# Performance work log

Hardware: AMD Instinct MI355X
Metric: run time of the kernel (lower is better)

Reference implementation:

```python
import jax, jax.numpy as jnp
import numpy as np

N_HEADS = 16

def setup_inputs() -> dict:
    key = jax.random.key(0)
    ks = jax.random.split(key, 8)
    bs, t, h, dh = 32, 512, 1024, 64
    s = lambda k, shape: jax.random.normal(k, shape, dtype=jnp.float32) * 0.02
    return {
        "x": jax.random.normal(ks[0], (bs, t, h), dtype=jnp.float32),
        "Wq": s(ks[1], (h, h)),
        "bq": s(ks[2], (h,)),
        "Wk": s(ks[3], (h, h)),
        "bk": s(ks[4], (h,)),
        "Wv": s(ks[5], (h, dh)),
        "bv": s(ks[6], (dh,)),
        "Wo": s(ks[7], (dh, h)),
    }

def reference(x, Wq, bq, Wk, bk, Wv, bv, Wo):
    bs, t, h = x.shape
    dh = Wv.shape[1]
    nh = N_HEADS
    # projections (context == x; static_features=None path)
    q = (x @ Wq + bq).reshape(bs, t, nh, dh)   # [b,t,h,d]
    k = (x @ Wk + bk).reshape(bs, t, nh, dh)
    v = x @ Wv + bv                             # shared single-head V: [b,t,d]
    scale = dh ** -0.5
    # per-head scores [b,h,q,k]
    score = jnp.einsum('bqhd,bkhd->bhqk', q, k) * scale
    # causal mask (mask_future_timesteps=True): -inf above diagonal
    mask = jnp.triu(jnp.full((t, t), -jnp.inf, dtype=score.dtype), 1)
    score = score + mask
    prob = jax.nn.softmax(score, axis=-1)       # attn_dropout is identity (p=0)
    # broadcast shared V across heads
    attn_vec = jnp.einsum('bhqk,bkd->bhqd', prob, v)   # [b,h,t,d]
    m_attn_vec = jnp.mean(attn_vec, axis=1)            # head-mean pooling [b,t,d]
    out = m_attn_vec @ Wo                              # out_proj, no bias; out_dropout identity
    return out, attn_vec
```

## Files before the change

### kernel.cpp

```cpp
#include <hip/hip_runtime.h>
#include <hip/hip_bf16.h>
#include <math.h>

#define BS 32
#define TT 512
#define HH 1024
#define NH 16
#define DH 64
#define MM (BS*TT)
#define NCAT 2176

typedef __attribute__((ext_vector_type(8))) __bf16 bf16x8;
typedef __attribute__((ext_vector_type(4))) float  f32x4;

#define QSCALE 0.18033688011112042f

__device__ __forceinline__ void gld16(const void* g, void* l) {
    __builtin_amdgcn_global_load_lds(
        (const __attribute__((address_space(1))) unsigned int*)g,
        (__attribute__((address_space(3))) unsigned int*)l,
        16, 0, 0);
}

__global__ __launch_bounds__(256) void cvt_x(const float* __restrict__ x,
                                             __bf16* __restrict__ xb)
{
    const size_t i = ((size_t)blockIdx.x * 256 + threadIdx.x) * 8;
    float4 a = *(const float4*)(x + i);
    float4 b = *(const float4*)(x + i + 4);
    bf16x8 v;
    v[0] = (__bf16)a.x; v[1] = (__bf16)a.y; v[2] = (__bf16)a.z; v[3] = (__bf16)a.w;
    v[4] = (__bf16)b.x; v[5] = (__bf16)b.y; v[6] = (__bf16)b.z; v[7] = (__bf16)b.w;
    *(bf16x8*)(xb + i) = v;
}

__global__ __launch_bounds__(256) void prep_w(
    const float* __restrict__ Wq, const float* __restrict__ Wk,
    const float* __restrict__ Wv, const float* __restrict__ bq_,
    const float* __restrict__ bk_, const float* __restrict__ bv_,
    __bf16* __restrict__ Wt, float* __restrict__ bias_cat)
{
    __shared__ __align__(16) __bf16 tile[64][72];
    const int tid = threadIdx.x;
    const int n0 = blockIdx.x * 64;
    const int k0 = blockIdx.y * 64;

    const int n_l = tid & 63;
    const int k_b = tid >> 6;
    const int n   = n0 + n_l;
    #pragma unroll
    for (int j = 0; j < 16; ++j) {
        const int k_l = j * 4 + k_b;
        const int k   = k0 + k_l;
        float v;
        if (n < 1024)      v = Wq[(size_t)k * 1024 + n];
        else if (n < 2048) v = Wk[(size_t)k * 1024 + (n - 1024)];
        else if (n < 2112) v = Wv[(size_t)k * 64 + (n - 2048)];
        else               v = 0.f;
        tile[n_l][k_l] = (__bf16)v;
    }
    if (blockIdx.y == 0 && tid < 64) {
        const int nn = n0 + tid;
        bias_cat[nn] = (nn < 1024) ? bq_[nn]
                     : (nn < 2048) ? bk_[nn - 1024]
                     : (nn < 2112) ? bv_[nn - 2048] : 0.f;
    }
    __syncthreads();
    const int n_l2 = tid >> 2;
    const int k_l2 = (tid & 3) * 16;
    __bf16* dst = Wt + (size_t)(n0 + n_l2) * 1024 + k0 + k_l2;
    *(bf16x8*)dst       = *(const bf16x8*)&tile[n_l2][k_l2];
    *(bf16x8*)(dst + 8) = *(const bf16x8*)&tile[n_l2][k_l2 + 8];
}

__global__ __launch_bounds__(256) void gemm_qkv(
    const __bf16* __restrict__ A, const __bf16* __restrict__ B,
    const float* __restrict__ bias_cat,
    __bf16* __restrict__ Qo, __bf16* __restrict__ Ko,
    __bf16* __restrict__ Vt)
{
    __shared__ __align__(16) __bf16 sA[128 * 32];
    __shared__ __align__(16) __bf16 sB[128 * 32];

    const int tid  = threadIdx.x;
    const int wv   = tid >> 6;
    const int ln   = tid & 63;
    const int quad = ln >> 4;
    const int l16  = ln & 15;
    const int m0 = blockIdx.y * 128;
    const int n0 = blockIdx.x * 128;

    const int rw = (wv & 1) * 64;
    const int cw = (wv >> 1) * 64;

    f32x4 acc[4][4];
    #pragma unroll
    for (int i = 0; i < 4; ++i)
        #pragma unroll
        for (int j = 0; j < 4; ++j) acc[i][j] = f32x4{0, 0, 0, 0};

    const int srow = wv * 16 + (ln >> 2);
    const int scol = (ln & 3) * 8;
    const __bf16* ga0 = A + (size_t)(m0 + srow) * 1024 + scol;
    const __bf16* gb0 = B + (size_t)(n0 + srow) * 1024 + scol;
    __bf16* la0 = sA + wv * 512;
    __bf16* lb0 = sB + wv * 512;

    for (int k0 = 0; k0 < 1024; k0 += 32) {
        gld16(ga0 + k0, la0);
        gld16(ga0 + (size_t)64 * 1024 + k0, la0 + 2048);
        gld16(gb0 + k0, lb0);
        gld16(gb0 + (size_t)64 * 1024 + k0, lb0 + 2048);
        __syncthreads();

        bf16x8 af[4], bfr[4];
        #pragma unroll
        for (int mt = 0; mt < 4; ++mt)
            af[mt] = *(const bf16x8*)&sA[(rw + mt * 16 + l16) * 32 + quad * 8];
        #pragma unroll
        for (int nt = 0; nt < 4; ++nt)
            bfr[nt] = *(const bf16x8*)&sB[(cw + nt * 16 + l16) * 32 + quad * 8];
        #pragma unroll
        for (int mt = 0; mt < 4; ++mt)
            #pragma unroll
            for (int nt = 0; nt < 4; ++nt)
                acc[mt][nt] = __builtin_amdgcn_mfma_f32_16x16x32_bf16(af[mt], bfr[nt], acc[mt][nt], 0, 0, 0);
        __syncthreads();
    }

    #pragma unroll
    for (int mt = 0; mt < 4; ++mt) {
        #pragma unroll
        for (int nt = 0; nt < 4; ++nt) {
            const int colb = n0 + cw + nt * 16 + l16;
            if (colb >= 2112) continue;
            const float bias = bias_cat[colb];
            #pragma unroll
            for (int r = 0; r < 4; ++r) {
                const int row = m0 + rw + mt * 16 + quad * 4 + r;
                const int b = row >> 9, t = row & 511;
                float v = acc[mt][nt][r] + bias;
                if (colb < 1024) {
                    const int h = colb >> 6, d = colb & 63;
                    Qo[(((size_t)(b * NH + h) * TT) + t) * DH + d] = (__bf16)(v * QSCALE);
                } else if (colb < 2048) {
                    const int c = colb - 1024;
                    const int h = c >> 6, d = c & 63;
                    Ko[(((size_t)(b * NH + h) * TT) + t) * DH + d] = (__bf16)v;
                } else {
                    const int d = colb - 2048;
                    Vt[((size_t)(b * DH + d)) * TT + t] = (__bf16)v;
                }
            }
        }
    }
}

__global__ __launch_bounds__(256) void zero_mav(float* __restrict__ p)
{
    ((float4*)p)[(size_t)blockIdx.x * 256 + threadIdx.x] = float4{0, 0, 0, 0};
}

__global__ __launch_bounds__(256) void attn_mfma(
    const __bf16* __restrict__ Q, const __bf16* __restrict__ K,
    const __bf16* __restrict__ Vt, float* __restrict__ attn_vec,
    float* __restrict__ mav)
{
    const int wave = threadIdx.x >> 6;
    const int lane = threadIdx.x & 63;
    const int wid  = blockIdx.x * 4 + wave;
    const int qt2  = wid & 15;
    const int bh   = wid >> 4;
    const int b    = bh >> 4;
    const int q0   = qt2 << 5;
    const int quad = lane >> 4;
    const int l16  = lane & 15;

    const __bf16* Qbh = Q  + (size_t)bh * TT * DH;
    const __bf16* Kbh = K  + (size_t)bh * TT * DH;
    const __bf16* Vb  = Vt + (size_t)b  * DH * TT;

    const bf16x8 qA_lo = *(const bf16x8*)(Qbh + (size_t)(q0 + l16) * DH + quad * 8);
    const bf16x8 qA_hi = *(const bf16x8*)(Qbh + (size_t)(q0 + l16) * DH + 32 + quad * 8);
    const bf16x8 qB_lo = *(const bf16x8*)(Qbh + (size_t)(q0 + 16 + l16) * DH + quad * 8);
    const bf16x8 qB_hi = *(const bf16x8*)(Qbh + (size_t)(q0 + 16 + l16) * DH + 32 + quad * 8);

    const int perm = ((l16 >> 2) << 3) + (l16 & 3);
    const __bf16* kp1 = Kbh + (size_t)perm * DH;
    const __bf16* kp2 = Kbh + (size_t)(perm + 4) * DH;

    f32x4 OA[4] = {f32x4{0,0,0,0}, f32x4{0,0,0,0}, f32x4{0,0,0,0}, f32x4{0,0,0,0}};
    f32x4 OB[4] = {f32x4{0,0,0,0}, f32x4{0,0,0,0}, f32x4{0,0,0,0}, f32x4{0,0,0,0}};
    float lA = 0.f, lB = 0.f;

    const int kend = q0 + 32;

    bf16x8 k1a = *(const bf16x8*)(kp1 + quad * 8);
    bf16x8 k1b = *(const bf16x8*)(kp1 + 32 + quad * 8);
    bf16x8 k2a = *(const bf16x8*)(kp2 + quad * 8);
    bf16x8 k2b = *(const bf16x8*)(kp2 + 32 + quad * 8);

    for (int kb0 = 0; kb0 < kend; kb0 += 32) {
        const __bf16* vp = Vb + (size_t)l16 * TT + kb0 + quad * 8;
        bf16x8 vf0 = *(const bf16x8*)(vp);
        bf16x8 vf1 = *(const bf16x8*)(vp + (size_t)16 * TT);
        bf16x8 vf2 = *(const bf16x8*)(vp + (size_t)32 * TT);
        bf16x8 vf3 = *(const bf16x8*)(vp + (size_t)48 * TT);

        f32x4 s1A = __builtin_amdgcn_mfma_f32_16x16x32_bf16(k1a, qA_lo, f32x4{0,0,0,0}, 0, 0, 0);
        s1A       = __builtin_amdgcn_mfma_f32_16x16x32_bf16(k1b, qA_hi, s1A, 0, 0, 0);
        f32x4 s2A = __builtin_amdgcn_mfma_f32_16x16x32_bf16(k2a, qA_lo, f32x4{0,0,0,0}, 0, 0, 0);
        s2A       = __builtin_amdgcn_mfma_f32_16x16x32_bf16(k2b, qA_hi, s2A, 0, 0, 0);
        f32x4 s1B = __builtin_amdgcn_mfma_f32_16x16x32_bf16(k1a, qB_lo, f32x4{0,0,0,0}, 0, 0, 0);
        s1B       = __builtin_amdgcn_mfma_f32_16x16x32_bf16(k1b, qB_hi, s1B, 0, 0, 0);
        f32x4 s2B = __builtin_amdgcn_mfma_f32_16x16x32_bf16(k2a, qB_lo, f32x4{0,0,0,0}, 0, 0, 0);
        s2B       = __builtin_amdgcn_mfma_f32_16x16x32_bf16(k2b, qB_hi, s2B, 0, 0, 0);

        {
            const int kbn = (kb0 + 32 < kend) ? kb0 + 32 : kb0;
            const __bf16* nk1 = kp1 + (size_t)kbn * DH;
            const __bf16* nk2 = kp2 + (size_t)kbn * DH;
            k1a = *(const bf16x8*)(nk1 + quad * 8);
            k1b = *(const bf16x8*)(nk1 + 32 + quad * 8);
            k2a = *(const bf16x8*)(nk2 + quad * 8);
            k2b = *(const bf16x8*)(nk2 + 32 + quad * 8);
        }

        if (kb0 == q0) {
            const int qqA = q0 + l16, qqB = q0 + 16 + l16;
            #pragma unroll
            for (int r = 0; r < 4; ++r) {
                const int key1 = kb0 + quad * 8 + r;
                const int key2 = key1 + 4;
                if (key1 > qqA) s1A[r] = -INFINITY;
                if (key2 > qqA) s2A[r] = -INFINITY;
                if (key1 > qqB) s1B[r] = -INFINITY;
                if (key2 > qqB) s2B[r] = -INFINITY;
            }
        }

        bf16x8 pfA, pfB;
        float psA = 0.f, psB = 0.f;
        #pragma unroll
        for (int r = 0; r < 4; ++r) {
            float pa0 = exp2f(s1A[r]);
            float pa1 = exp2f(s2A[r]);
            float pb0 = exp2f(s1B[r]);
            float pb1 = exp2f(s2B[r]);
            psA += pa0 + pa1;
            psB += pb0 + pb1;
            pfA[r]     = (__bf16)pa0;
            pfA[4 + r] = (__bf16)pa1;
            pfB[r]     = (__bf16)pb0;
            pfB[4 + r] = (__bf16)pb1;
        }
        lA += psA;
        lB += psB;

        OA[0] = __builtin_amdgcn_mfma_f32_16x16x32_bf16(pfA, vf0, OA[0], 0, 0, 0);
        OB[0] = __builtin_amdgcn_mfma_f32_16x16x32_bf16(pfB, vf0, OB[0], 0, 0, 0);
        OA[1] = __builtin_amdgcn_mfma_f32_16x16x32_bf16(pfA, vf1, OA[1], 0, 0, 0);
        OB[1] = __builtin_amdgcn_mfma_f32_16x16x32_bf16(pfB, vf1, OB[1], 0, 0, 0);
        OA[2] = __builtin_amdgcn_mfma_f32_16x16x32_bf16(pfA, vf2, OA[2], 0, 0, 0);
        OB[2] = __builtin_amdgcn_mfma_f32_16x16x32_bf16(pfB, vf2, OB[2], 0, 0, 0);
        OA[3] = __builtin_amdgcn_mfma_f32_16x16x32_bf16(pfA, vf3, OA[3], 0, 0, 0);
        OB[3] = __builtin_amdgcn_mfma_f32_16x16x32_bf16(pfB, vf3, OB[3], 0, 0, 0);
    }

    lA += __shfl_xor(lA, 16);
    lA += __shfl_xor(lA, 32);
    lB += __shfl_xor(lB, 16);
    lB += __shfl_xor(lB, 32);

    #pragma unroll
    for (int r = 0; r < 4; ++r) {
        const float invA = 1.0f / __shfl(lA, quad * 4 + r);
        const float invB = 1.0f / __shfl(lB, quad * 4 + r);
        const int tA = q0 + quad * 4 + r;
        const int tB = tA + 16;
        float* opA = attn_vec + ((size_t)bh * TT + tA) * DH + l16;
        float* opB = attn_vec + ((size_t)bh * TT + tB) * DH + l16;
        float* mpA = mav + ((size_t)(b * TT + tA)) * DH + l16;
        float* mpB = mav + ((size_t)(b * TT + tB)) * DH + l16;
        #pragma unroll
        for (int nt = 0; nt < 4; ++nt) {
            const float vA = OA[nt][r] * invA;
            const float vB = OB[nt][r] * invB;
            opA[nt * 16] = vA;
            opB[nt * 16] = vB;
            atomicAdd(mpA + nt * 16, vA * (1.f / 16.f));
            atomicAdd(mpB + nt * 16, vB * (1.f / 16.f));
        }
    }
}

__global__ __launch_bounds__(256) void gemm_out(
    const float* __restrict__ A, const float* __restrict__ B,
    float* __restrict__ C, int M, int N, int K)
{
    __shared__ __align__(16) __bf16 sA[64][32];
    __shared__ __align__(16) __bf16 sB[64][32];

    const int tid  = threadIdx.x;
    const int wave = tid >> 6;
    const int lane = tid & 63;
    const int m0 = blockIdx.y * 64;
    const int n0 = blockIdx.x * 64;

    f32x4 acc[4] = {f32x4{0,0,0,0}, f32x4{0,0,0,0}, f32x4{0,0,0,0}, f32x4{0,0,0,0}};

    const int ar = tid >> 2;
    const int ac = (tid & 3) * 8;
    const int bk = tid >> 3;
    const int bc = (tid & 7) * 8;
    const int quad = lane >> 4;
    const int l16  = lane & 15;

    for (int k0 = 0; k0 < K; k0 += 32) {
        const float* ap = A + (size_t)(m0 + ar) * K + k0 + ac;
        float4 a0 = *(const float4*)ap;
        float4 a1 = *(const float4*)(ap + 4);
        {
            bf16x8 av;
            av[0] = (__bf16)a0.x; av[1] = (__bf16)a0.y; av[2] = (__bf16)a0.z; av[3] = (__bf16)a0.w;
            av[4] = (__bf16)a1.x; av[5] = (__bf16)a1.y; av[6] = (__bf16)a1.z; av[7] = (__bf16)a1.w;
            *(bf16x8*)&sA[ar][ac] = av;
        }
        const float* bp = B + (size_t)(k0 + bk) * N + n0 + bc;
        float4 b0 = *(const float4*)bp;
        float4 b1 = *(const float4*)(bp + 4);
        sB[bc + 0][bk] = (__bf16)b0.x;
        sB[bc + 1][bk] = (__bf16)b0.y;
        sB[bc + 2][bk] = (__bf16)b0.z;
        sB[bc + 3][bk] = (__bf16)b0.w;
        sB[bc + 4][bk] = (__bf16)b1.x;
        sB[bc + 5][bk] = (__bf16)b1.y;
        sB[bc + 6][bk] = (__bf16)b1.z;
        sB[bc + 7][bk] = (__bf16)b1.w;
        __syncthreads();

        bf16x8 afrag = *(const bf16x8*)&sA[wave * 16 + l16][quad * 8];
        #pragma unroll
        for (int tn = 0; tn < 4; ++tn) {
            bf16x8 bfrag = *(const bf16x8*)&sB[tn * 16 + l16][quad * 8];
            acc[tn] = __builtin_amdgcn_mfma_f32_16x16x32_bf16(afrag, bfrag, acc[tn], 0, 0, 0);
        }
        __syncthreads();
    }

    #pragma unroll
    for (int tn = 0; tn < 4; ++tn) {
        #pragma unroll
        for (int r = 0; r < 4; ++r) {
            int row = m0 + wave * 16 + quad * 4 + r;
            int col = n0 + tn * 16 + l16;
            C[(size_t)row * N + col] = acc[tn][r];
        }
    }
}

extern "C" void kernel_launch(void* const* d_in, const int* in_sizes, int n_in,
                              void* d_out, int out_size, void* d_ws, size_t ws_size,
                              hipStream_t stream)
{
    const float* x  = (const float*)d_in[0];
    const float* Wq = (const float*)d_in[1];
    const float* bq = (const float*)d_in[2];
    const float* Wk = (const float*)d_in[3];
    const float* bk = (const float*)d_in[4];
    const float* Wv = (const float*)d_in[5];
    const float* bv = (const float*)d_in[6];
    const float* Wo = (const float*)d_in[7];

    float* out      = (float*)d_out;
    float* attn_vec = out + (size_t)MM * HH;

    char* ws = (char*)d_ws;
    __bf16* xb  = (__bf16*)ws;
    __bf16* Wt  = xb + (size_t)MM * HH;
    float* bias_cat = (float*)(Wt + (size_t)NCAT * HH);
    __bf16* Qb  = (__bf16*)(bias_cat + 2304);
    __bf16* Kb  = Qb + (size_t)MM * HH;
    __bf16* Vt  = Kb + (size_t)MM * HH;
    float*  mav = (float*)xb;

    cvt_x<<<MM * HH / (256 * 8), 256, 0, stream>>>(x, xb);
    prep_w<<<dim3(NCAT / 64, HH / 64), 256, 0, stream>>>(Wq, Wk, Wv, bq, bk, bv, Wt, bias_cat);
    gemm_qkv<<<dim3(NCAT / 128, MM / 128), 256, 0, stream>>>(xb, Wt, bias_cat, Qb, Kb, Vt);
    zero_mav<<<(MM * DH / 4) / 256, 256, 0, stream>>>(mav);
    attn_mfma<<<(BS * NH * TT / 32) / 4, 256, 0, stream>>>(Qb, Kb, Vt, attn_vec, mav);
    gemm_out<<<dim3(HH / 64, MM / 64), 256, 0, stream>>>(mav, Wo, out, MM, HH, DH);
}
```

Baseline: 437.2 us.

## Reduce head-mean in shared memory with all heads per block, pair causal tiles

The attention kernel now launches one 1024-thread block per (batch, tile pair), with 16 waves covering the 16 heads. Each wave processes two query tiles, q-tile p and 15-p, to balance causal work. The head-mean is accumulated with LDS atomics into a shared buffer and written once with plain stores, so the zero_mav kernel and the global atomics go away. In exchange, the grid has fewer, larger blocks (256 blocks of 1024 threads), which may hurt occupancy and latency hiding. Each wave also now runs its two tiles one after the other.

```diff
diff --git a/kernel.cpp b/kernel.cpp
--- a/kernel.cpp
+++ b/kernel.cpp
@@ -156,141 +156,162 @@
     }
 }
 
-__global__ __launch_bounds__(256) void zero_mav(float* __restrict__ p)
-{
-    ((float4*)p)[(size_t)blockIdx.x * 256 + threadIdx.x] = float4{0, 0, 0, 0};
-}
-
-__global__ __launch_bounds__(256) void attn_mfma(
+__global__ __launch_bounds__(1024) void attn_mfma(
     const __bf16* __restrict__ Q, const __bf16* __restrict__ K,
     const __bf16* __restrict__ Vt, float* __restrict__ attn_vec,
     float* __restrict__ mav)
 {
+    __shared__ float smav[64][65];
+
     const int wave = threadIdx.x >> 6;
     const int lane = threadIdx.x & 63;
-    const int wid  = blockIdx.x * 4 + wave;
-    const int qt2  = wid & 15;
-    const int bh   = wid >> 4;
-    const int b    = bh >> 4;
-    const int q0   = qt2 << 5;
+    const int pair = blockIdx.x & 7;
+    const int b    = blockIdx.x >> 3;
+    const int bh   = b * NH + wave;
     const int quad = lane >> 4;
     const int l16  = lane & 15;
+
+    {
+        float* p = &smav[0][0];
+        for (int i = threadIdx.x; i < 64 * 65; i += 1024) p[i] = 0.f;
+    }
+    __syncthreads();
 
     const __bf16* Qbh = Q  + (size_t)bh * TT * DH;
     const __bf16* Kbh = K  + (size_t)bh * TT * DH;
     const __bf16* Vb  = Vt + (size_t)b  * DH * TT;
 
-    const bf16x8 qA_lo = *(const bf16x8*)(Qbh + (size_t)(q0 + l16) * DH + quad * 8);
-    const bf16x8 qA_hi = *(const bf16x8*)(Qbh + (size_t)(q0 + l16) * DH + 32 + quad * 8);
-    const bf16x8 qB_lo = *(const bf16x8*)(Qbh + (size_t)(q0 + 16 + l16) * DH + quad * 8);
-    const bf16x8 qB_hi = *(const bf16x8*)(Qbh + (size_t)(q0 + 16 + l16) * DH + 32 + quad * 8);
-
     const int perm = ((l16 >> 2) << 3) + (l16 & 3);
     const __bf16* kp1 = Kbh + (size_t)perm * DH;
     const __bf16* kp2 = Kbh + (size_t)(perm + 4) * DH;
 
-    f32x4 OA[4] = {f32x4{0,0,0,0}, f32x4{0,0,0,0}, f32x4{0,0,0,0}, f32x4{0,0,0,0}};
-    f32x4 OB[4] = {f32x4{0,0,0,0}, f32x4{0,0,0,0}, f32x4{0,0,0,0}, f32x4{0,0,0,0}};
-    float lA = 0.f, lB = 0.f;
-
-    const int kend = q0 + 32;
-
-    bf16x8 k1a = *(const bf16x8*)(kp1 + quad * 8);
-    bf16x8 k1b = *(const bf16x8*)(kp1 + 32 + quad * 8);
-    bf16x8 k2a = *(const bf16x8*)(kp2 + quad * 8);
-    bf16x8 k2b = *(const bf16x8*)(kp2 + 32 + quad * 8);
-
-    for (int kb0 = 0; kb0 < kend; kb0 += 32) {
-        const __bf16* vp = Vb + (size_t)l16 * TT + kb0 + quad * 8;
-        bf16x8 vf0 = *(const bf16x8*)(vp);
-        bf16x8 vf1 = *(const bf16x8*)(vp + (size_t)16 * TT);
-        bf16x8 vf2 = *(const bf16x8*)(vp + (size_t)32 * TT);
-        bf16x8 vf3 = *(const bf16x8*)(vp + (size_t)48 * TT);
-
-        f32x4 s1A = __builtin_amdgcn_mfma_f32_16x16x32_bf16(k1a, qA_lo, f32x4{0,0,0,0}, 0, 0, 0);
-        s1A       = __builtin_amdgcn_mfma_f32_16x16x32_bf16(k1b, qA_hi, s1A, 0, 0, 0);
-        f32x4 s2A = __builtin_amdgcn_mfma_f32_16x16x32_bf16(k2a, qA_lo, f32x4{0,0,0,0}, 0, 0, 0);
-        s2A       = __builtin_amdgcn_mfma_f32_16x16x32_bf16(k2b, qA_hi, s2A, 0, 0, 0);
-        f32x4 s1B = __builtin_amdgcn_mfma_f32_16x16x32_bf16(k1a, qB_lo, f32x4{0,0,0,0}, 0, 0, 0);
-        s1B       = __builtin_amdgcn_mfma_f32_16x16x32_bf16(k1b, qB_hi, s1B, 0, 0, 0);
-        f32x4 s2B = __builtin_amdgcn_mfma_f32_16x16x32_bf16(k2a, qB_lo, f32x4{0,0,0,0}, 0, 0, 0);
-        s2B       = __builtin_amdgcn_mfma_f32_16x16x32_bf16(k2b, qB_hi, s2B, 0, 0, 0);
-
-        {
-            const int kbn = (kb0 + 32 < kend) ? kb0 + 32 : kb0;
-            const __bf16* nk1 = kp1 + (size_t)kbn * DH;
-            const __bf16* nk2 = kp2 + (size_t)kbn * DH;
-            k1a = *(const bf16x8*)(nk1 + quad * 8);
-            k1b = *(const bf16x8*)(nk1 + 32 + quad * 8);
-            k2a = *(const bf16x8*)(nk2 + quad * 8);
-            k2b = *(const bf16x8*)(nk2 + 32 + quad * 8);
-        }
-
-        if (kb0 == q0) {
-            const int qqA = q0 + l16, qqB = q0 + 16 + l16;
+    #pragma unroll 1
+    for (int rep = 0; rep < 2; ++rep) {
+        const int qt2 = rep ? (15 - pair) : pair;
+        const int q0  = qt2 << 5;
+        const int kend = q0 + 32;
+
+        const bf16x8 qA_lo = *(const bf16x8*)(Qbh + (size_t)(q0 + l16) * DH + quad * 8);
+        const bf16x8 qA_hi = *(const bf16x8*)(Qbh + (size_t)(q0 + l16) * DH + 32 + quad * 8);
+        const bf16x8 qB_lo = *(const bf16x8*)(Qbh + (size_t)(q0 + 16 + l16) * DH + quad * 8);
+        const bf16x8 qB_hi = *(const bf16x8*)(Qbh + (size_t)(q0 + 16 + l16) * DH + 32 + quad * 8);
+
+        f32x4 OA[4] = {f32x4{0,0,0,0}, f32x4{0,0,0,0}, f32x4{0,0,0,0}, f32x4{0,0,0,0}};
+        f32x4 OB[4] = {f32x4{0,0,0,0}, f32x4{0,0,0,0}, f32x4{0,0,0,0}, f32x4{0,0,0,0}};
+        float lA = 0.f, lB = 0.f;
+
+        bf16x8 k1a = *(const bf16x8*)(kp1 + quad * 8);
+        bf16x8 k1b = *(const bf16x8*)(kp1 + 32 + quad * 8);
+        bf16x8 k2a = *(const bf16x8*)(kp2 + quad * 8);
+        bf16x8 k2b = *(const bf16x8*)(kp2 + 32 + quad * 8);
+
+        for (int kb0 = 0; kb0 < kend; kb0 += 32) {
+            const __bf16* vp = Vb + (size_t)l16 * TT + kb0 + quad * 8;
+            bf16x8 vf0 = *(const bf16x8*)(vp);
+            bf16x8 vf1 = *(const bf16x8*)(vp + (size_t)16 * TT);
+            bf16x8 vf2 = *(const bf16x8*)(vp + (size_t)32 * TT);
+            bf16x8 vf3 = *(const bf16x8*)(vp + (size_t)48 * TT);
+
+            f32x4 s1A = __builtin_amdgcn_mfma_f32_16x16x32_bf16(k1a, qA_lo, f32x4{0,0,0,0}, 0, 0, 0);
+            s1A       = __builtin_amdgcn_mfma_f32_16x16x32_bf16(k1b, qA_hi, s1A, 0, 0, 0);
+            f32x4 s2A = __builtin_amdgcn_mfma_f32_16x16x32_bf16(k2a, qA_lo, f32x4{0,0,0,0}, 0, 0, 0);
+            s2A       = __builtin_amdgcn_mfma_f32_16x16x32_bf16(k2b, qA_hi, s2A, 0, 0, 0);
+            f32x4 s1B = __builtin_amdgcn_mfma_f32_16x16x32_bf16(k1a, qB_lo, f32x4{0,0,0,0}, 0, 0, 0);
+            s1B       = __builtin_amdgcn_mfma_f32_16x16x32_bf16(k1b, qB_hi, s1B, 0, 0, 0);
+            f32x4 s2B = __builtin_amdgcn_mfma_f32_16x16x32_bf16(k2a, qB_lo, f32x4{0,0,0,0}, 0, 0, 0);
+            s2B       = __builtin_amdgcn_mfma_f32_16x16x32_bf16(k2b, qB_hi, s2B, 0, 0, 0);
+
+            {
+                const int kbn = (kb0 + 32 < kend) ? kb0 + 32 : kb0;
+                const __bf16* nk1 = kp1 + (size_t)kbn * DH;
+                const __bf16* nk2 = kp2 + (size_t)kbn * DH;
+                k1a = *(const bf16x8*)(nk1 + quad * 8);
+                k1b = *(const bf16x8*)(nk1 + 32 + quad * 8);
+                k2a = *(const bf16x8*)(nk2 + quad * 8);
+                k2b = *(const bf16x8*)(nk2 + 32 + quad * 8);
+            }
+
+            if (kb0 == q0) {
+                const int qqA = q0 + l16, qqB = q0 + 16 + l16;
+                #pragma unroll
+                for (int r = 0; r < 4; ++r) {
+                    const int key1 = kb0 + quad * 8 + r;
+                    const int key2 = key1 + 4;
+                    if (key1 > qqA) s1A[r] = -INFINITY;
+                    if (key2 > qqA) s2A[r] = -INFINITY;
+                    if (key1 > qqB) s1B[r] = -INFINITY;
+                    if (key2 > qqB) s2B[r] = -INFINITY;
+                }
+            }
+
+            bf16x8 pfA, pfB;
+            float psA = 0.f, psB = 0.f;
             #pragma unroll
             for (int r = 0; r < 4; ++r) {
-                const int key1 = kb0 + quad * 8 + r;
-                const int key2 = key1 + 4;
-                if (key1 > qqA) s1A[r] = -INFINITY;
-                if (key2 > qqA) s2A[r] = -INFINITY;
-                if (key1 > qqB) s1B[r] = -INFINITY;
-                if (key2 > qqB) s2B[r] = -INFINITY;
+                float pa0 = exp2f(s1A[r]);
+                float pa1 = exp2f(s2A[r]);
+                float pb0 = exp2f(s1B[r]);
+                float pb1 = exp2f(s2B[r]);
+                psA += pa0 + pa1;
+                psB += pb0 + pb1;
+                pfA[r]     = (__bf16)pa0;
+                pfA[4 + r] = (__bf16)pa1;
+                pfB[r]     = (__bf16)pb0;
+                pfB[4 + r] = (__bf16)pb1;
             }
-        }
-
-        bf16x8 pfA, pfB;
-        float psA = 0.f, psB = 0.f;
+            lA += psA;
+            lB += psB;
+
+            OA[0] = __builtin_amdgcn_mfma_f32_16x16x32_bf16(pfA, vf0, OA[0], 0, 0, 0);
+            OB[0] = __builtin_amdgcn_mfma_f32_16x16x32_bf16(pfB, vf0, OB[0], 0, 0, 0);
+            OA[1] = __builtin_amdgcn_mfma_f32_16x16x32_bf16(pfA, vf1, OA[1], 0, 0, 0);
+            OB[1] = __builtin_amdgcn_mfma_f32_16x16x32_bf16(pfB, vf1, OB[1], 0, 0, 0);
+            OA[2] = __builtin_amdgcn_mfma_f32_16x16x32_bf16(pfA, vf2, OA[2], 0, 0, 0);
+            OB[2] = __builtin_amdgcn_mfma_f32_16x16x32_bf16(pfB, vf2, OB[2], 0, 0, 0);
+            OA[3] = __builtin_amdgcn_mfma_f32_16x16x32_bf16(pfA, vf3, OA[3], 0, 0, 0);
+            OB[3] = __builtin_amdgcn_mfma_f32_16x16x32_bf16(pfB, vf3, OB[3], 0, 0, 0);
+        }
+
+        lA += __shfl_xor(lA, 16);
+        lA += __shfl_xor(lA, 32);
+        lB += __shfl_xor(lB, 16);
+        lB += __shfl_xor(lB, 32);
+
         #pragma unroll
         for (int r = 0; r < 4; ++r) {
-            float pa0 = exp2f(s1A[r]);
-            float pa1 = exp2f(s2A[r]);
-            float pb0 = exp2f(s1B[r]);
-            float pb1 = exp2f(s2B[r]);
-            psA += pa0 + pa1;
-            psB += pb0 + pb1;
-            pfA[r]     = (__bf16)pa0;
-            pfA[4 + r] = (__bf16)pa1;
-            pfB[r]     = (__bf16)pb0;
-            pfB[4 + r] = (__bf16)pb1;
-        }
-        lA += psA;
-        lB += psB;
-
-        OA[0] = __builtin_amdgcn_mfma_f32_16x16x32_bf16(pfA, vf0, OA[0], 0, 0, 0);
-        OB[0] = __builtin_amdgcn_mfma_f32_16x16x32_bf16(pfB, vf0, OB[0], 0, 0, 0);
-        OA[1] = __builtin_amdgcn_mfma_f32_16x16x32_bf16(pfA, vf1, OA[1], 0, 0, 0);
-        OB[1] = __builtin_amdgcn_mfma_f32_16x16x32_bf16(pfB, vf1, OB[1], 0, 0, 0);
-        OA[2] = __builtin_amdgcn_mfma_f32_16x16x32_bf16(pfA, vf2, OA[2], 0, 0, 0);
-        OB[2] = __builtin_amdgcn_mfma_f32_16x16x32_bf16(pfB, vf2, OB[2], 0, 0, 0);
-        OA[3] = __builtin_amdgcn_mfma_f32_16x16x32_bf16(pfA, vf3, OA[3], 0, 0, 0);
-        OB[3] = __builtin_amdgcn_mfma_f32_16x16x32_bf16(pfB, vf3, OB[3], 0, 0, 0);
-    }
-
-    lA += __shfl_xor(lA, 16);
-    lA += __shfl_xor(lA, 32);
-    lB += __shfl_xor(lB, 16);
-    lB += __shfl_xor(lB, 32);
-
-    #pragma unroll
-    for (int r = 0; r < 4; ++r) {
-        const float invA = 1.0f / __shfl(lA, quad * 4 + r);
-        const float invB = 1.0f / __shfl(lB, quad * 4 + r);
-        const int tA = q0 + quad * 4 + r;
-        const int tB = tA + 16;
-        float* opA = attn_vec + ((size_t)bh * TT + tA) * DH + l16;
-        float* opB = attn_vec + ((size_t)bh * TT + tB) * DH + l16;
-        float* mpA = mav + ((size_t)(b * TT + tA)) * DH + l16;
-        float* mpB = mav + ((size_t)(b * TT + tB)) * DH + l16;
-        #pragma unroll
-        for (int nt = 0; nt < 4; ++nt) {
-            const float vA = OA[nt][r] * invA;
-            const float vB = OB[nt][r] * invB;
-            opA[nt * 16] = vA;
-            opB[nt * 16] = vB;
-            atomicAdd(mpA + nt * 16, vA * (1.f / 16.f));
-            atomicAdd(mpB + nt * 16, vB * (1.f / 16.f));
-        }
+            const float invA = 1.0f / __shfl(lA, quad * 4 + r);
+            const float invB = 1.0f / __shfl(lB, quad * 4 + r);
+            const int tA = q0 + quad * 4 + r;
+            const int tB = tA + 16;
+            const int ltA = rep * 32 + quad * 4 + r;
+            const int ltB = ltA + 16;
+            float* opA = attn_vec + ((size_t)bh * TT + tA) * DH + l16;
+            float* opB = attn_vec + ((size_t)bh * TT + tB) * DH + l16;
+            #pragma unroll
+            for (int nt = 0; nt < 4; ++nt) {
+                const float vA = OA[nt][r] * invA;
+                const float vB = OB[nt][r] * invB;
+                opA[nt * 16] = vA;
+                opB[nt * 16] = vB;
+                atomicAdd(&smav[ltA][nt * 16 + l16], vA * (1.f / 16.f));
+                atomicAdd(&smav[ltB][nt * 16 + l16], vB * (1.f / 16.f));
+            }
+        }
+    }
+
+    __syncthreads();
+
+    {
+        const int row = threadIdx.x >> 4;
+        const int d0  = (threadIdx.x & 15) * 4;
+        const int t   = (row < 32) ? ((pair << 5) + row)
+                                   : (((15 - pair) << 5) + (row - 32));
+        float4 v;
+        v.x = smav[row][d0];
+        v.y = smav[row][d0 + 1];
+        v.z = smav[row][d0 + 2];
+        v.w = smav[row][d0 + 3];
+        *(float4*)(mav + ((size_t)(b * TT + t)) * DH + d0) = v;
     }
 }
 
@@ -387,7 +408,6 @@
     cvt_x<<<MM * HH / (256 * 8), 256, 0, stream>>>(x, xb);
     prep_w<<<dim3(NCAT / 64, HH / 64), 256, 0, stream>>>(Wq, Wk, Wv, bq, bk, bv, Wt, bias_cat);
     gemm_qkv<<<dim3(NCAT / 128, MM / 128), 256, 0, stream>>>(xb, Wt, bias_cat, Qb, Kb, Vt);
-    zero_mav<<<(MM * DH / 4) / 256, 256, 0, stream>>>(mav);
-    attn_mfma<<<(BS * NH * TT / 32) / 4, 256, 0, stream>>>(Qb, Kb, Vt, attn_vec, mav);
+    attn_mfma<<<BS * 8, 1024, 0, stream>>>(Qb, Kb, Vt, attn_vec, mav);
     gemm_out<<<dim3(HH / 64, MM / 64), 256, 0, stream>>>(mav, Wo, out, MM, HH, DH);
 }
```

Measured after the change: 436.6 us. Within noise of the previous version (-0.1%).
